# Performance work log

Hardware: AMD Instinct MI355X
Metric: run time of the kernel (lower is better)

## Reference

```python
import jax, jax.numpy as jnp
import numpy as np

B, D, H = 4096, 32, 1024  # batch, in_out_dim, hidden width


def setup_inputs() -> dict:
    key = jax.random.key(0)
    ks = jax.random.split(key, 10)

    def lin_w(k, shape, fan_in):
        bound = 1.0 / np.sqrt(fan_in)
        return jax.random.uniform(k, shape, jnp.float32, -bound, bound)

    return {
        "t": jax.random.uniform(ks[0], (1,), jnp.float32),
        "z": jax.random.normal(ks[1], (B, D), jnp.float32),
        "W0": lin_w(ks[2], (H, D + 1), D + 1),
        "b0": lin_w(ks[3], (H,), D + 1),
        "W1": lin_w(ks[4], (H, H), H),
        "b1": lin_w(ks[5], (H,), H),
        "W2": lin_w(ks[6], (H, H), H),
        "b2": lin_w(ks[7], (H,), H),
        "W3": lin_w(ks[8], (D, H), H),
        "b3": lin_w(ks[9], (D,), H),
    }


def _mlp(v, params):
    # Linear -> Tanh chain, final Linear (torch convention y = x @ W.T + b)
    for W, b in params[:-1]:
        v = jnp.tanh(v @ W.T + b)
    W, b = params[-1]
    return v @ W.T + b


def reference(t, z, W0, b0, W1, b1, W2, b2, W3, b3):
    bsz, d = z.shape
    tt = jnp.broadcast_to(t.reshape(-1), (bsz,))  # check_t: repeat scalar t
    params = [(W0, b0), (W1, b1), (W2, b2), (W3, b3)]

    def f(zz):  # [B, D] -> [B, D]
        v = jnp.concatenate([zz, tt[:, None]], axis=1)  # [B, D+1]
        return _mlp(v, params)

    out = f(z)

    # Exact Jacobian trace via d forward-mode JVPs (replaces the per-dim
    # autograd.grad loop in trace_df_dz with a single vmapped JVP batch).
    eye = jnp.eye(d, dtype=z.dtype)

    def jvp_i(e):
        return jax.jvp(f, (z,), (jnp.broadcast_to(e, z.shape),))[1]  # [B, D]

    tang = jax.vmap(jvp_i)(eye)            # [D, B, D]
    trace = jnp.einsum("ibi->b", tang)     # sum_i df_i/dz_i per sample
    divv = -trace
    return out, divv[:, None]
```

## Files before the change

kernel.cpp:

```cpp
#include <hip/hip_runtime.h>
#include <hip/hip_bf16.h>
#include <stdint.h>


using bf  = __hip_bfloat16;
using bf2 = __hip_bfloat162;
typedef __attribute__((ext_vector_type(8))) short bf16x8;
typedef __attribute__((ext_vector_type(4))) float f32x4;

__device__ __forceinline__ float b2f(bf x)    { return __bfloat162float(x); }
__device__ __forceinline__ bf    f2b(float x) { return __float2bfloat16(x); }

__device__ __forceinline__ void gld16(const void* g, void* l) {
  __builtin_amdgcn_global_load_lds((const __attribute__((address_space(1))) void*)g,
                                   (__attribute__((address_space(3))) void*)l,
                                   16, 0, 0);
}

__device__ __forceinline__ void conv_body(int blk, const float* __restrict__ src,
                                          bf* __restrict__ dst, int n4) {
  const int i = blk * 256 + threadIdx.x;
  if (i >= n4) return;
  float4 v = ((const float4*)src)[i];
  bf2* d = (bf2*)(dst + (size_t)i * 4);
  d[0] = __float22bfloat162_rn(make_float2(v.x, v.y));
  d[1] = __float22bfloat162_rn(make_float2(v.z, v.w));
}

__device__ __forceinline__ void w0t_body(int blk, const float* __restrict__ W0,
                                         bf* __restrict__ W0T) {
  const int idx = blk * 256 + threadIdx.x;
  const int i = idx >> 10, q = idx & 1023;
  W0T[idx] = f2b(W0[q * 33 + i]);
}

__global__ __launch_bounds__(256) void prep_k(const float* __restrict__ z,
                                              const float* __restrict__ tin,
                                              const float* __restrict__ W0,
                                              const float* __restrict__ b0,
                                              const float* __restrict__ W1,
                                              const float* __restrict__ W2,
                                              const float* __restrict__ W3,
                                              bf* __restrict__ h0,
                                              bf* __restrict__ W0T,
                                              bf* __restrict__ W1b,
                                              bf* __restrict__ W2b,
                                              bf* __restrict__ W3b,
                                              float* __restrict__ out2) {
  __shared__ float zs[32 * 33];
  const int f = blockIdx.x, t = threadIdx.x;
  if (f < 128) {
    const int s0 = f * 32;
    for (int j = t; j < 1024; j += 256) {
      const int s = j >> 5, k = j & 31;
      zs[s * 33 + k] = z[(size_t)(s0 + s) * 32 + k];
    }
    if (t < 32) zs[t * 33 + 32] = tin[0];
    __syncthreads();
#pragma unroll 1
    for (int rep = 0; rep < 4; ++rep) {
      const int hh = rep * 256 + t;
      const float* wr = W0 + (size_t)hh * 33;
      float wv[33];
#pragma unroll
      for (int k = 0; k < 33; ++k) wv[k] = wr[k];
      const float bv = b0[hh];
#pragma unroll 1
      for (int s = 0; s < 32; ++s) {
        float acc = bv;
#pragma unroll
        for (int k = 0; k < 33; ++k) acc += wv[k] * zs[s * 33 + k];
        h0[(size_t)(s0 + s) * 1024 + hh] = f2b(tanhf(acc));
      }
    }
  } else if (f < 1152) {
    conv_body(f - 128, W1, W1b, 262144);
  } else if (f < 2176) {
    conv_body(f - 1152, W2, W2b, 262144);
  } else if (f < 2208) {
    conv_body(f - 2176, W3, W3b, 8192);
  } else if (f < 2336) {
    w0t_body(f - 2208, W0, W0T);
  } else {
#pragma unroll
    for (int u = 0; u < 16; ++u) out2[u * 256 + t] = 0.f;
  }
}

template <int MF>
__device__ __forceinline__ void gemm_core(bf* As, bf* Bs,
                                          const bf* __restrict__ A,
                                          const bf* __restrict__ B,
                                          size_t m0, size_t n0,
                                          f32x4 (&acc)[MF][4]) {
  constexpr int K = 1024;
  const int t = threadIdx.x, l = t & 63, w = t >> 6;
  const int wm = w >> 1, wn = w & 1;
  const int r15 = l & 15, q4 = l >> 4, sw = r15 & 7;

  const int lrow = l >> 3;
  const int lseg = (l & 7) ^ lrow;
  const bf* asrc[MF]; bf* alds[MF];
  const bf* bsrc[4]; bf* blds[4];
#pragma unroll
  for (int u = 0; u < MF; ++u) {
    const int row = w * (MF * 8) + u * 8 + lrow;
    asrc[u] = A + (m0 + row) * K + lseg * 8;
    alds[u] = As + (size_t)(w * (MF * 8) + u * 8) * 64;
  }
#pragma unroll
  for (int u = 0; u < 4; ++u) {
    const int row = w * 32 + u * 8 + lrow;
    bsrc[u] = B + (n0 + row) * K + lseg * 8;
    blds[u] = Bs + (size_t)(w * 32 + u * 8) * 64;
  }

#pragma unroll 1
  for (int k0 = 0; k0 < K; k0 += 64) {
#pragma unroll
    for (int u = 0; u < MF; ++u) gld16(asrc[u] + k0, alds[u]);
#pragma unroll
    for (int u = 0; u < 4; ++u) gld16(bsrc[u] + k0, blds[u]);
    __syncthreads();
#pragma unroll
    for (int kk = 0; kk < 2; ++kk) {
      const int sa = (kk * 4 + q4) ^ sw;
      bf16x8 af[MF], bfr[4];
#pragma unroll
      for (int i = 0; i < MF; ++i)
        af[i] = *(const bf16x8*)(As + (wm * (MF * 16) + i * 16 + r15) * 64 + sa * 8);
#pragma unroll
      for (int j = 0; j < 4; ++j)
        bfr[j] = *(const bf16x8*)(Bs + (wn * 64 + j * 16 + r15) * 64 + sa * 8);
#pragma unroll
      for (int mi = 0; mi < MF; ++mi)
#pragma unroll
        for (int ni = 0; ni < 4; ++ni)
          acc[mi][ni] = __builtin_amdgcn_mfma_f32_16x16x32_bf16(af[mi], bfr[ni], acc[mi][ni], 0, 0, 0);
    }
    __syncthreads();
  }
}

__global__ __launch_bounds__(256, 2) void gemm_fwd(const bf* __restrict__ A,
                                                   const bf* __restrict__ W,
                                                   const float* __restrict__ bias,
                                                   bf* __restrict__ H) {
  constexpr int N = 1024;
  __shared__ __align__(16) bf As[128 * 64];
  __shared__ __align__(16) bf Bs[128 * 64];
  const int t = threadIdx.x, l = t & 63, w = t >> 6;
  const int wm = w >> 1, wn = w & 1;
  const int f = blockIdx.x;
  const int n_t = (f >> 3) & 7, m_t = (f & 7) + 8 * (f >> 6);
  const size_t m0 = (size_t)m_t * 128, n0 = (size_t)n_t * 128;
  const int r15 = l & 15, q4 = l >> 4;
  f32x4 acc[4][4] = {};
  gemm_core<4>(As, Bs, A, W, m0, n0, acc);
#pragma unroll
  for (int ni = 0; ni < 4; ++ni) {
    const int n = (int)n0 + wn * 64 + ni * 16 + r15;
    const float bv = bias[n];
#pragma unroll
    for (int mi = 0; mi < 4; ++mi)
#pragma unroll
      for (int r = 0; r < 4; ++r) {
        const size_t m = m0 + wm * 64 + mi * 16 + q4 * 4 + r;
        H[m * N + n] = f2b(tanhf(acc[mi][ni][r] + bv));
      }
  }
}

__global__ __launch_bounds__(256) void fwd3_k(const bf* __restrict__ h2,
                                              const bf* __restrict__ W3b,
                                              const float* __restrict__ b3,
                                              float* __restrict__ out) {
  __shared__ __align__(16) bf hs[8 * 1024];
  const int t = threadIdx.x;
  const size_t bb = (size_t)blockIdx.x * 8;
  const uint4* src = (const uint4*)(h2 + bb * 1024);
  uint4* dv = (uint4*)hs;
#pragma unroll
  for (int j = 0; j < 4; ++j) dv[j * 256 + t] = src[j * 256 + t];
  __syncthreads();
  const int i = t & 31, bl = t >> 5;
  const bf2* hr = (const bf2*)(hs + bl * 1024);
  const bf2* wr = (const bf2*)(W3b + (size_t)i * 1024);
  float s = 0.f;
#pragma unroll 8
  for (int k2 = 0; k2 < 512; ++k2) {
    float2 a = __bfloat1622float2(hr[k2]);
    float2 c = __bfloat1622float2(wr[k2]);
    s += a.x * c.x + a.y * c.y;
  }
  out[(bb + bl) * 32 + i] = s + b3[i];
}

__global__ __launch_bounds__(256) void t0_k(const bf* __restrict__ h0c,
                                            const bf* __restrict__ W0T,
                                            bf* __restrict__ T0) {
  const int idx = blockIdx.x * 256 + threadIdx.x;
  const int m = idx >> 6, seg = idx & 63;
  const int b = m >> 5, i = m & 31;
  const bf2* hp = (const bf2*)(h0c + (size_t)b * 1024 + seg * 16);
  const bf2* wp = (const bf2*)(W0T + (size_t)i * 1024 + seg * 16);
  bf2* dp = (bf2*)(T0 + (size_t)m * 1024 + seg * 16);
#pragma unroll
  for (int u = 0; u < 8; ++u) {
    float2 h = __bfloat1622float2(hp[u]);
    float2 w = __bfloat1622float2(wp[u]);
    float2 r;
    r.x = (1.f - h.x * h.x) * w.x;
    r.y = (1.f - h.y * h.y) * w.y;
    dp[u] = __float22bfloat162_rn(r);
  }
}

__global__ __launch_bounds__(256, 2) void gemm_jvp1(const bf* __restrict__ T0,
                                                    const bf* __restrict__ W1b,
                                                    const bf* __restrict__ h1c,
                                                    bf* __restrict__ T1) {
  constexpr int N = 1024;
  __shared__ __align__(16) bf As[256 * 64];
  __shared__ __align__(16) bf Bs[128 * 64];
  const int t = threadIdx.x, l = t & 63, w = t >> 6;
  const int wm = w >> 1, wn = w & 1;
  const int f = blockIdx.x;
  const int n_t = (f >> 3) & 7, m_t = (f & 7) + 8 * (f >> 6);
  const size_t m0 = (size_t)m_t * 256, n0 = (size_t)n_t * 128;
  const int r15 = l & 15, q4 = l >> 4;
  f32x4 acc[8][4] = {};
  gemm_core<8>(As, Bs, T0, W1b, m0, n0, acc);
  const int bbase = (int)((m0 + wm * 128) >> 5);
#pragma unroll
  for (int ni = 0; ni < 4; ++ni) {
    const int n = (int)n0 + wn * 64 + ni * 16 + r15;
    float a1v[4];
#pragma unroll
    for (int s = 0; s < 4; ++s) {
      const float hv = b2f(h1c[(size_t)(bbase + s) * 1024 + n]);
      a1v[s] = 1.f - hv * hv;
    }
#pragma unroll
    for (int mi = 0; mi < 8; ++mi)
#pragma unroll
      for (int r = 0; r < 4; ++r) {
        const size_t m = m0 + wm * 128 + mi * 16 + q4 * 4 + r;
        T1[m * N + n] = f2b(a1v[mi >> 1] * acc[mi][ni][r]);
      }
  }
}

__global__ __launch_bounds__(256, 2) void gemm_jvp2(const bf* __restrict__ T1,
                                                    const bf* __restrict__ W2b,
                                                    const bf* __restrict__ W3b,
                                                    const bf* __restrict__ h2c,
                                                    float* __restrict__ out2c) {
  __shared__ __align__(16) bf As[256 * 64];
  __shared__ __align__(16) bf Bs[128 * 64];
  const int t = threadIdx.x, l = t & 63, w = t >> 6;
  const int wm = w >> 1, wn = w & 1;
  const int f = blockIdx.x;
  const int n_t = (f >> 3) & 7, m_t = (f & 7) + 8 * (f >> 6);
  const size_t m0 = (size_t)m_t * 256, n0 = (size_t)n_t * 128;
  const int r15 = l & 15, q4 = l >> 4;
  f32x4 acc[8][4] = {};
  gemm_core<8>(As, Bs, T1, W2b, m0, n0, acc);
  const int bbase = (int)((m0 + wm * 128) >> 5);
  float part[4] = {0.f, 0.f, 0.f, 0.f};
#pragma unroll
  for (int ni = 0; ni < 4; ++ni) {
    const int n = (int)n0 + wn * 64 + ni * 16 + r15;
    float a2v[4];
#pragma unroll
    for (int s = 0; s < 4; ++s) {
      const float hv = b2f(h2c[(size_t)(bbase + s) * 1024 + n]);
      a2v[s] = 1.f - hv * hv;
    }
#pragma unroll
    for (int mi = 0; mi < 8; ++mi) {
      const int isel = mi >> 1;
#pragma unroll
      for (int r = 0; r < 4; ++r) {
        const int mm = wm * 128 + mi * 16 + q4 * 4 + r;
        part[isel] += b2f(W3b[(size_t)(mm & 31) * 1024 + n]) * a2v[isel] * acc[mi][ni][r];
      }
    }
  }
#pragma unroll
  for (int off = 32; off > 0; off >>= 1) {
#pragma unroll
    for (int s = 0; s < 4; ++s) part[s] += __shfl_down(part[s], off);
  }
  if (l == 0) {
#pragma unroll
    for (int s = 0; s < 4; ++s) atomicAdd(out2c + bbase + s, -part[s]);
  }
}

extern "C" void kernel_launch(void* const* d_in, const int* in_sizes, int n_in,
                              void* d_out, int out_size, void* d_ws, size_t ws_size,
                              hipStream_t stream) {
  const float* tin = (const float*)d_in[0];
  const float* z   = (const float*)d_in[1];
  const float* W0  = (const float*)d_in[2];
  const float* b0  = (const float*)d_in[3];
  const float* W1  = (const float*)d_in[4];
  const float* b1  = (const float*)d_in[5];
  const float* W2  = (const float*)d_in[6];
  const float* b2  = (const float*)d_in[7];
  const float* W3  = (const float*)d_in[8];
  const float* b3  = (const float*)d_in[9];
  float* out = (float*)d_out;
  float* out2 = out + 131072;
  (void)in_sizes; (void)n_in; (void)out_size;

  char* ws = (char*)d_ws;
  size_t off = 0;
  auto take = [&](size_t bytes) {
    char* p = ws + off;
    off = (off + bytes + 255) & ~(size_t)255;
    return p;
  };
  bf* h0   = (bf*)take((size_t)4096 * 1024 * 2);
  bf* h1   = (bf*)take((size_t)4096 * 1024 * 2);
  bf* h2   = (bf*)take((size_t)4096 * 1024 * 2);
  bf* W0T  = (bf*)take((size_t)32 * 1024 * 2);
  bf* W1b  = (bf*)take((size_t)1024 * 1024 * 2);
  bf* W2b  = (bf*)take((size_t)1024 * 1024 * 2);
  bf* W3b  = (bf*)take((size_t)32 * 1024 * 2);
  const size_t avail = (ws_size > off) ? (ws_size - off) : 0;
  int NB = 4096;
  while (NB > 256 && 2 * (size_t)NB * 65536 > avail) NB >>= 1;
  bf* T0 = (bf*)take((size_t)NB * 65536);
  bf* T1 = (bf*)take((size_t)NB * 65536);

  prep_k<<<dim3(2337), dim3(256), 0, stream>>>(z, tin, W0, b0, W1, W2, W3,
                                               h0, W0T, W1b, W2b, W3b, out2);
  gemm_fwd<<<dim3(256), dim3(256), 0, stream>>>(h0, W1b, b1, h1);
  gemm_fwd<<<dim3(256), dim3(256), 0, stream>>>(h1, W2b, b2, h2);
  fwd3_k<<<dim3(512), dim3(256), 0, stream>>>(h2, W3b, b3, out);
  for (int cb = 0; cb < 4096; cb += NB) {
    t0_k<<<dim3(NB * 8), dim3(256), 0, stream>>>(h0 + (size_t)cb * 1024, W0T, T0);
    gemm_jvp1<<<dim3(NB), dim3(256), 0, stream>>>(
        T0, W1b, h1 + (size_t)cb * 1024, T1);
    gemm_jvp2<<<dim3(NB), dim3(256), 0, stream>>>(
        T1, W2b, W3b, h2 + (size_t)cb * 1024, out2 + cb);
  }
}
```

Baseline: 803.9 us.

## Fuse T0 tangent construction into first JVP GEMM prologue

Removes the separate t0_k kernel that materialized the [B*32,1024] T0 tangent matrix in global memory. The first JVP GEMM now builds its A tile on the fly from h0 and W0T, computing (1-h^2)*W0T into swizzled LDS each k-step, while W1 tiles still stream in via global_load_lds. This avoids writing and re-reading a large bf16 buffer, and halves workspace use so chunks can be larger. In exchange the A-side load is no longer asynchronous, and elementwise math plus register loads now sit in the GEMM main loop.

```diff
diff --git a/kernel.cpp b/kernel.cpp
--- a/kernel.cpp
+++ b/kernel.cpp
@@ -10,6 +10,9 @@
 
 __device__ __forceinline__ float b2f(bf x)    { return __bfloat162float(x); }
 __device__ __forceinline__ bf    f2b(float x) { return __float2bfloat16(x); }
+__device__ __forceinline__ float s2f(short s) {
+  return __uint_as_float(((unsigned)(unsigned short)s) << 16);
+}
 
 __device__ __forceinline__ void gld16(const void* g, void* l) {
   __builtin_amdgcn_global_load_lds((const __attribute__((address_space(1))) void*)g,
@@ -196,31 +199,12 @@
   out[(bb + bl) * 32 + i] = s + b3[i];
 }
 
-__global__ __launch_bounds__(256) void t0_k(const bf* __restrict__ h0c,
-                                            const bf* __restrict__ W0T,
-                                            bf* __restrict__ T0) {
-  const int idx = blockIdx.x * 256 + threadIdx.x;
-  const int m = idx >> 6, seg = idx & 63;
-  const int b = m >> 5, i = m & 31;
-  const bf2* hp = (const bf2*)(h0c + (size_t)b * 1024 + seg * 16);
-  const bf2* wp = (const bf2*)(W0T + (size_t)i * 1024 + seg * 16);
-  bf2* dp = (bf2*)(T0 + (size_t)m * 1024 + seg * 16);
-#pragma unroll
-  for (int u = 0; u < 8; ++u) {
-    float2 h = __bfloat1622float2(hp[u]);
-    float2 w = __bfloat1622float2(wp[u]);
-    float2 r;
-    r.x = (1.f - h.x * h.x) * w.x;
-    r.y = (1.f - h.y * h.y) * w.y;
-    dp[u] = __float22bfloat162_rn(r);
-  }
-}
-
-__global__ __launch_bounds__(256, 2) void gemm_jvp1(const bf* __restrict__ T0,
-                                                    const bf* __restrict__ W1b,
-                                                    const bf* __restrict__ h1c,
-                                                    bf* __restrict__ T1) {
-  constexpr int N = 1024;
+__global__ __launch_bounds__(256, 2) void gemm_jvp1f(const bf* __restrict__ h0c,
+                                                     const bf* __restrict__ W0T,
+                                                     const bf* __restrict__ W1b,
+                                                     const bf* __restrict__ h1c,
+                                                     bf* __restrict__ T1) {
+  constexpr int K = 1024;
   __shared__ __align__(16) bf As[256 * 64];
   __shared__ __align__(16) bf Bs[128 * 64];
   const int t = threadIdx.x, l = t & 63, w = t >> 6;
@@ -228,9 +212,84 @@
   const int f = blockIdx.x;
   const int n_t = (f >> 3) & 7, m_t = (f & 7) + 8 * (f >> 6);
   const size_t m0 = (size_t)m_t * 256, n0 = (size_t)n_t * 128;
-  const int r15 = l & 15, q4 = l >> 4;
+  const int r15 = l & 15, q4 = l >> 4, sw = r15 & 7;
+  const int lrow = l >> 3, kseg = l & 7;
+  const int lseg = kseg ^ lrow;
+
+  const bf* bsrc[4]; bf* blds[4];
+#pragma unroll
+  for (int u = 0; u < 4; ++u) {
+    const int row = w * 32 + u * 8 + lrow;
+    bsrc[u] = W1b + (n0 + row) * K + lseg * 8;
+    blds[u] = Bs + (size_t)(w * 32 + u * 8) * 64;
+  }
+
+  const int b0 = (int)(m0 >> 5);
+  const bf* hp0 = h0c + (size_t)(b0 + 2 * w) * K + kseg * 8;
+  const bf* hp1 = hp0 + K;
+  const bf* wp[4];
+#pragma unroll
+  for (int j = 0; j < 4; ++j) wp[j] = W0T + (size_t)(lrow + 8 * j) * K + kseg * 8;
+  bf* awr[8];
+#pragma unroll
+  for (int u = 0; u < 8; ++u)
+    awr[u] = As + (size_t)(w * 64 + u * 8 + lrow) * 64 + lseg * 8;
+
   f32x4 acc[8][4] = {};
-  gemm_core<8>(As, Bs, T0, W1b, m0, n0, acc);
+  bf16x8 hv0 = *(const bf16x8*)hp0;
+  bf16x8 hv1 = *(const bf16x8*)hp1;
+  bf16x8 wv[4];
+#pragma unroll
+  for (int j = 0; j < 4; ++j) wv[j] = *(const bf16x8*)wp[j];
+
+#pragma unroll 1
+  for (int k0 = 0; k0 < K; k0 += 64) {
+#pragma unroll
+    for (int u = 0; u < 4; ++u) gld16(bsrc[u] + k0, blds[u]);
+    float a[2][8];
+#pragma unroll
+    for (int e = 0; e < 8; ++e) {
+      const float h0v = s2f(hv0[e]);
+      const float h1v = s2f(hv1[e]);
+      a[0][e] = 1.f - h0v * h0v;
+      a[1][e] = 1.f - h1v * h1v;
+    }
+#pragma unroll
+    for (int u = 0; u < 8; ++u) {
+      const bf16x8 wvu = wv[u & 3];
+      const float* aa = a[u >> 2];
+      union { bf2 b[4]; uint4 u4; } o;
+#pragma unroll
+      for (int p = 0; p < 4; ++p)
+        o.b[p] = __float22bfloat162_rn(make_float2(aa[2 * p] * s2f(wvu[2 * p]),
+                                                   aa[2 * p + 1] * s2f(wvu[2 * p + 1])));
+      *(uint4*)awr[u] = o.u4;
+    }
+    const int kn = (k0 + 64) & (K - 1);
+    hv0 = *(const bf16x8*)(hp0 + kn);
+    hv1 = *(const bf16x8*)(hp1 + kn);
+#pragma unroll
+    for (int j = 0; j < 4; ++j) wv[j] = *(const bf16x8*)(wp[j] + kn);
+    __syncthreads();
+#pragma unroll
+    for (int kk = 0; kk < 2; ++kk) {
+      const int sa = (kk * 4 + q4) ^ sw;
+      bf16x8 af[8], bfr[4];
+#pragma unroll
+      for (int i = 0; i < 8; ++i)
+        af[i] = *(const bf16x8*)(As + (wm * 128 + i * 16 + r15) * 64 + sa * 8);
+#pragma unroll
+      for (int j = 0; j < 4; ++j)
+        bfr[j] = *(const bf16x8*)(Bs + (wn * 64 + j * 16 + r15) * 64 + sa * 8);
+#pragma unroll
+      for (int mi = 0; mi < 8; ++mi)
+#pragma unroll
+        for (int ni = 0; ni < 4; ++ni)
+          acc[mi][ni] = __builtin_amdgcn_mfma_f32_16x16x32_bf16(af[mi], bfr[ni], acc[mi][ni], 0, 0, 0);
+    }
+    __syncthreads();
+  }
+
   const int bbase = (int)((m0 + wm * 128) >> 5);
 #pragma unroll
   for (int ni = 0; ni < 4; ++ni) {
@@ -246,7 +305,7 @@
 #pragma unroll
       for (int r = 0; r < 4; ++r) {
         const size_t m = m0 + wm * 128 + mi * 16 + q4 * 4 + r;
-        T1[m * N + n] = f2b(a1v[mi >> 1] * acc[mi][ni][r]);
+        T1[m * 1024 + n] = f2b(a1v[mi >> 1] * acc[mi][ni][r]);
       }
   }
 }
@@ -331,8 +390,7 @@
   bf* W3b  = (bf*)take((size_t)32 * 1024 * 2);
   const size_t avail = (ws_size > off) ? (ws_size - off) : 0;
   int NB = 4096;
-  while (NB > 256 && 2 * (size_t)NB * 65536 > avail) NB >>= 1;
-  bf* T0 = (bf*)take((size_t)NB * 65536);
+  while (NB > 256 && (size_t)NB * 65536 > avail) NB >>= 1;
   bf* T1 = (bf*)take((size_t)NB * 65536);
 
   prep_k<<<dim3(2337), dim3(256), 0, stream>>>(z, tin, W0, b0, W1, W2, W3,
@@ -341,9 +399,8 @@
   gemm_fwd<<<dim3(256), dim3(256), 0, stream>>>(h1, W2b, b2, h2);
   fwd3_k<<<dim3(512), dim3(256), 0, stream>>>(h2, W3b, b3, out);
   for (int cb = 0; cb < 4096; cb += NB) {
-    t0_k<<<dim3(NB * 8), dim3(256), 0, stream>>>(h0 + (size_t)cb * 1024, W0T, T0);
-    gemm_jvp1<<<dim3(NB), dim3(256), 0, stream>>>(
-        T0, W1b, h1 + (size_t)cb * 1024, T1);
+    gemm_jvp1f<<<dim3(NB), dim3(256), 0, stream>>>(
+        h0 + (size_t)cb * 1024, W0T, W1b, h1 + (size_t)cb * 1024, T1);
     gemm_jvp2<<<dim3(NB), dim3(256), 0, stream>>>(
         T1, W2b, W3b, h2 + (size_t)cb * 1024, out2 + cb);
   }
```

Result: faster. 731.9 us, median of 2 (-9.0%).
